# Performance work log

Hardware: AMD Instinct MI355X
Metric: run time of the kernel (lower is better)

Reference implementation:

```python
import jax, jax.numpy as jnp
import numpy as np

N = 50000      # nodes
E = 500000     # edges
MUL = 32       # multiplicity of 0e and 1o in node irreps
NUM_NEIGHBORS = 10.0
MIX = 0.15
INV3 = 1.0 / np.sqrt(3.0)  # sqrt(2*l3+1)*wigner_3j(1,1,0) = delta_ij/sqrt(3)


def setup_inputs() -> dict:
    key = jax.random.key(0)
    ks = jax.random.split(key, 16)
    f32 = jnp.float32
    node_input = jax.random.normal(ks[0], (N, 128), dtype=f32)  # 32x0e (32) + 32x1o (96)
    # edge_attr = spherical harmonics lmax=1, component normalization: Y0=1, |Y1|=sqrt(3)
    y1 = jax.random.normal(ks[1], (E, 3), dtype=f32)
    y1 = jnp.sqrt(3.0) * y1 / jnp.linalg.norm(y1, axis=1, keepdims=True)
    edge_attr = jnp.concatenate([jnp.ones((E, 1), f32), y1], axis=1)  # [E,4]
    edge_scalars = jax.random.uniform(ks[2], (E, 8), dtype=f32)       # radial embedding
    edge_src = jax.random.randint(ks[3], (E,), 0, N)
    edge_dst = jax.random.randint(ks[4], (E,), 0, N)
    rn = lambda k, s: jax.random.normal(k, s, dtype=f32)
    return {
        "node_input": node_input, "edge_attr": edge_attr, "edge_scalars": edge_scalars,
        "W1_s": rn(ks[5], (MUL, 2 * MUL)),  # first Linear, 0e block: 32 -> 64 (=feat 32 + self 32)
        "W1_v": rn(ks[6], (MUL, 2 * MUL)),  # first Linear, 1o block
        "M0": rn(ks[7], (8, 32)), "M1": rn(ks[8], (32, 32)),  # weight MLP (fc_neurons=[32,32])
        "Wtp0": rn(ks[9], (32, MUL)),   # path 0e x 0e -> 0e
        "Wtp1": rn(ks[10], (32, MUL)),  # path 0e x 1o -> 1o
        "Wtp2": rn(ks[11], (32, MUL)),  # path 1o x 0e -> 1o
        "Wtp3": rn(ks[12], (32, MUL)),  # path 1o x 1o -> 0e
        "W2_s": rn(ks[13], (2 * MUL, MUL)),  # final Linear, 0e: 64 -> 32
        "W2_v": rn(ks[14], (2 * MUL, MUL)),  # final Linear, 1o: 64 -> 32
        "edge_src": edge_src, "edge_dst": edge_dst,
    }


def _forward(node_input, edge_attr, edge_scalars, W1_s, W1_v, M0, M1,
             Wtp0, Wtp1, Wtp2, Wtp3, W2_s, W2_v, edge_src, edge_dst):
    n = node_input.shape[0]
    s = node_input[:, :MUL]                       # [N,32]  0e
    v = node_input[:, MUL:].reshape(n, MUL, 3)    # [N,32,3] 1o
    # Linear(node_input.irreps + irreps_out): per-irrep mixing, fan-in normalized
    s_all = (s @ W1_s) / jnp.sqrt(jnp.float32(MUL))                    # [N,64]
    v_all = jnp.einsum('nuk,uw->nwk', v, W1_v) / jnp.sqrt(jnp.float32(MUL))  # [N,64,3]
    feat_s, self_s = s_all[:, :MUL], s_all[:, MUL:]
    feat_v, self_v = v_all[:, :MUL], v_all[:, MUL:]

    # gather by edge source
    es = feat_s[edge_src]   # [E,32]
    ev = feat_v[edge_src]   # [E,32,3]
    y0 = edge_attr[:, 0]    # [E]
    y1 = edge_attr[:, 1:4]  # [E,3]

    # MLP on edge scalars -> per-edge, per-path 'uvu' weights (fan-in normalized)
    h = jax.nn.gelu(edge_scalars @ M0 / jnp.sqrt(jnp.float32(8)))
    h = jax.nn.gelu(h @ M1 / jnp.sqrt(jnp.float32(32)))                # [E,32]
    inv_sqrt_h = 1.0 / jnp.sqrt(jnp.float32(32))
    w0 = (h @ Wtp0) * inv_sqrt_h  # [E,32]
    w1 = (h @ Wtp1) * inv_sqrt_h
    w2 = (h @ Wtp2) * inv_sqrt_h
    w3 = (h @ Wtp3) * inv_sqrt_h

    # per-edge CG tensor product (4 'uvu' instructions)
    out0a = w0 * es * y0[:, None]                                    # 0e x 0e -> 0e
    out0b = w3 * jnp.einsum('euk,ek->eu', ev, y1) * INV3             # 1o x 1o -> 0e
    out1a = w1[:, :, None] * es[:, :, None] * y1[:, None, :]        # 0e x 1o -> 1o
    out1b = w2[:, :, None] * ev * y0[:, None, None]                 # 1o x 0e -> 1o
    out0 = jnp.concatenate([out0a, out0b], axis=1)                  # [E,64]  64x0e
    out1 = jnp.concatenate([out1a, out1b], axis=1)                  # [E,64,3] 64x1o

    # scatter-add to destination nodes, normalize by sqrt(num_neighbors)
    inv_deg = 1.0 / jnp.sqrt(jnp.float32(NUM_NEIGHBORS))
    ns = jax.ops.segment_sum(out0, edge_dst, num_segments=n) * inv_deg              # [N,64]
    nv = jax.ops.segment_sum(out1.reshape(-1, 2 * MUL * 3), edge_dst,
                             num_segments=n).reshape(n, 2 * MUL, 3) * inv_deg       # [N,64,3]

    # final per-irrep Linear to output irreps 32x0e + 32x1o
    conv_s = (ns @ W2_s) / jnp.sqrt(jnp.float32(2 * MUL))
    conv_v = jnp.einsum('nuk,uw->nwk', nv, W2_v) / jnp.sqrt(jnp.float32(2 * MUL))

    a = jnp.sqrt(jnp.float32(1.0 - MIX))
    b = jnp.sqrt(jnp.float32(MIX))
    out_s = a * self_s + b * conv_s                                  # [N,32]
    out_v = (a * self_v + b * conv_v).reshape(n, MUL * 3)            # [N,96]
    return jnp.concatenate([out_s, out_v], axis=1)                   # [N,128]


def reference(node_input, edge_attr, edge_scalars, W1_s, W1_v, M0, M1,
              Wtp0, Wtp1, Wtp2, Wtp3, W2_s, W2_v, edge_src, edge_dst):
    return _forward(node_input, edge_attr, edge_scalars, W1_s, W1_v, M0, M1,
                    Wtp0, Wtp1, Wtp2, Wtp3, W2_s, W2_v, edge_src, edge_dst)
```

## Files before the change

### kernel.cpp

```cpp
#include <hip/hip_runtime.h>
#include <math.h>

#define N_NODES 50000
#define N_EDGES 500000
#define NPB 16
#define GROUPS 8

__device__ __forceinline__ float gelu_fast(float x) {
    const float k0 = 0.7978845608028654f;
    const float k1 = 0.044715f;
    float z2 = 2.f * k0 * (x + k1 * x * x * x);
    float ez = __expf(z2);
    float th = 1.f - 2.f * __builtin_amdgcn_rcpf(ez + 1.f);
    return 0.5f * x * (1.f + th);
}

__device__ __forceinline__ unsigned short f2bf(float x) {
    unsigned int u = __float_as_uint(x);
    unsigned int r = (u + 0x7FFFu + ((u >> 16) & 1u)) >> 16;
    return (unsigned short)r;
}
__device__ __forceinline__ unsigned int pack2bf(float a, float b) {
    return (unsigned int)f2bf(a) | ((unsigned int)f2bf(b) << 16);
}
__device__ __forceinline__ float bf_lo(unsigned int w) {
    return __uint_as_float(w << 16);
}
__device__ __forceinline__ float bf_hi(unsigned int w) {
    return __uint_as_float(w & 0xffff0000u);
}

__device__ __forceinline__ void lds_add(float* p, float v) {
    unsigned int off = (unsigned int)(size_t)p;
    asm volatile("ds_add_f32 %0, %1" :: "v"(off), "v"(v) : "memory");
}

__global__ void node_pre(const float* __restrict__ node_input,
                         const float* __restrict__ W1_s,
                         const float* __restrict__ W1_v,
                         float* __restrict__ feat,
                         float* __restrict__ out) {
    __shared__ float lWs[32 * 64];
    __shared__ float lWv[32 * 64];
    for (int i = threadIdx.x; i < 2048; i += blockDim.x) {
        lWs[i] = W1_s[i];
        lWv[i] = W1_v[i];
    }
    __syncthreads();
    int n = blockIdx.x * blockDim.x + threadIdx.x;
    if (n >= N_NODES) return;
    const float inv_sqrt_mul = 0.17677669529663687f;
    const float a_mix = 0.9219544457292887f;

    float s[32];
#pragma unroll
    for (int u = 0; u < 32; ++u) s[u] = node_input[n * 128 + u];
#pragma unroll 4
    for (int w = 0; w < 64; ++w) {
        float acc = 0.f;
#pragma unroll
        for (int u = 0; u < 32; ++u) acc += s[u] * lWs[u * 64 + w];
        acc *= inv_sqrt_mul;
        if (w < 32) feat[(size_t)n * 128 + w * 4 + 0] = acc;
        else        out[n * 128 + (w - 32)] = a_mix * acc;
    }
#pragma unroll
    for (int k = 0; k < 3; ++k) {
        float vk[32];
#pragma unroll
        for (int u = 0; u < 32; ++u) vk[u] = node_input[n * 128 + 32 + u * 3 + k];
#pragma unroll 4
        for (int w = 0; w < 64; ++w) {
            float acc = 0.f;
#pragma unroll
            for (int u = 0; u < 32; ++u) acc += vk[u] * lWv[u * 64 + w];
            acc *= inv_sqrt_mul;
            if (w < 32) feat[(size_t)n * 128 + w * 4 + 1 + k] = acc;
            else        out[n * 128 + 32 + (w - 32) * 3 + k] = a_mix * acc;
        }
    }
}

__global__ void hist_kernel(const int* __restrict__ edge_dst, int* __restrict__ counts) {
    int e = blockIdx.x * blockDim.x + threadIdx.x;
    if (e < N_EDGES) atomicAdd(&counts[edge_dst[e]], 1);
}

__global__ void scan_kernel(const int* __restrict__ counts,
                            int* __restrict__ offsets,
                            int* __restrict__ cursor) {
    const int T = 1024;
    __shared__ int partial[T];
    int t = threadIdx.x;
    const int chunk = (N_NODES + T - 1) / T;
    int start = t * chunk;
    int end = start + chunk; if (end > N_NODES) end = N_NODES;
    if (start > N_NODES) start = N_NODES;
    int sum = 0;
    for (int i = start; i < end; ++i) sum += counts[i];
    partial[t] = sum;
    __syncthreads();
    for (int off = 1; off < T; off <<= 1) {
        int other = (t >= off) ? partial[t - off] : 0;
        __syncthreads();
        partial[t] += other;
        __syncthreads();
    }
    int run = (t == 0) ? 0 : partial[t - 1];
    for (int i = start; i < end; ++i) {
        offsets[i] = run;
        cursor[i] = run;
        run += counts[i];
    }
    if (t == T - 1) offsets[N_NODES] = run;
}

__global__ void scatter_kernel(const int* __restrict__ edge_src,
                               const int* __restrict__ edge_dst,
                               const float* __restrict__ edge_attr,
                               int* __restrict__ cursor,
                               float4* __restrict__ ySorted,
                               int4* __restrict__ sde) {
    int e = blockIdx.x * blockDim.x + threadIdx.x;
    if (e >= N_EDGES) return;
    int d = edge_dst[e];
    int pos = atomicAdd(&cursor[d], 1);
    ySorted[pos] = *(const float4*)(edge_attr + (size_t)e * 4);
    sde[pos] = make_int4(edge_src[e], d, e, 0);
}

__global__ void __launch_bounds__(256)
h_kernel(const float* __restrict__ edge_scalars,
         const float* __restrict__ M0,
         const float* __restrict__ M1,
         uint4* __restrict__ hOut) {
    __shared__ unsigned int stage[256 * 20];

    const int wv   = threadIdx.x >> 6;
    const int lane = threadIdx.x & 63;
    const int e0w  = blockIdx.x * 256 + wv * 64;
    int e = e0w + lane;
    int ec = e < N_EDGES ? e : N_EDGES - 1;

    const float inv_sqrt8  = 0.35355339059327373f;
    const float inv_sqrt32 = 0.17677669529663687f;

    const float4 s0 = *(const float4*)(edge_scalars + (size_t)ec * 8);
    const float4 s1 = *(const float4*)(edge_scalars + (size_t)ec * 8 + 4);

    float t[32];
#pragma unroll
    for (int u = 0; u < 32; ++u) {
        float acc = s0.x * M0[0 * 32 + u] + s0.y * M0[1 * 32 + u]
                  + s0.z * M0[2 * 32 + u] + s0.w * M0[3 * 32 + u]
                  + s1.x * M0[4 * 32 + u] + s1.y * M0[5 * 32 + u]
                  + s1.z * M0[6 * 32 + u] + s1.w * M0[7 * 32 + u];
        t[u] = gelu_fast(acc * inv_sqrt8);
    }
    float h[32];
#pragma unroll
    for (int u = 0; u < 32; ++u) {
        float acc = 0.f;
#pragma unroll
        for (int m = 0; m < 32; ++m) acc += t[m] * M1[m * 32 + u];
        h[u] = gelu_fast(acc * inv_sqrt32);
    }

    unsigned int* myrow = stage + threadIdx.x * 20;
#pragma unroll
    for (int c = 0; c < 4; ++c) {
        uint4 pk;
        pk.x = pack2bf(h[c * 8 + 0], h[c * 8 + 1]);
        pk.y = pack2bf(h[c * 8 + 2], h[c * 8 + 3]);
        pk.z = pack2bf(h[c * 8 + 4], h[c * 8 + 5]);
        pk.w = pack2bf(h[c * 8 + 6], h[c * 8 + 7]);
        *(uint4*)&myrow[c * 4] = pk;
    }
    asm volatile("s_waitcnt lgkmcnt(0)" ::: "memory");
#pragma unroll
    for (int p = 0; p < 4; ++p) {
        const int el = p * 16 + (lane >> 2);
        const int c  = lane & 3;
        const uint4 v = *(const uint4*)&stage[(wv * 64 + el) * 20 + c * 4];
        const int ge = e0w + el;
        if (ge < N_EDGES)
            hOut[(size_t)ge * 4 + c] = v;
    }
}

__global__ void __launch_bounds__(256)
conv_kernel(const uint4* __restrict__ hBuf,
            const float4* __restrict__ ySorted,
            const int4* __restrict__ sde,
            const int* __restrict__ offsets,
            const float* __restrict__ Wtp0,
            const float* __restrict__ Wtp1,
            const float* __restrict__ Wtp2,
            const float* __restrict__ Wtp3,
            const float* __restrict__ W2_s,
            const float* __restrict__ W2_v,
            const float* __restrict__ feat,
            float* __restrict__ out) {
    __shared__ float sacc[NPB * 256];
    for (int i = threadIdx.x; i < NPB * 256; i += blockDim.x) sacc[i] = 0.f;

    const int lane = threadIdx.x & 31;
    const int g = threadIdx.x >> 5;

    const float inv_sqrt32 = 0.17677669529663687f;
    unsigned int wA[32], wB[32];
#pragma unroll
    for (int j = 0; j < 32; ++j) {
        wA[j] = pack2bf(Wtp0[j * 32 + lane] * inv_sqrt32,
                        Wtp1[j * 32 + lane] * inv_sqrt32);
        wB[j] = pack2bf(Wtp2[j * 32 + lane] * inv_sqrt32,
                        Wtp3[j * 32 + lane] * inv_sqrt32);
    }
    __syncthreads();

    const int n0 = blockIdx.x * NPB;
    const int eb = offsets[n0];
    const int ee = offsets[n0 + NPB];
    const float INV3 = 0.5773502691896258f;
    const float4* feat4 = (const float4*)feat;

    const int total = ee - eb;
    const int per = (total + GROUPS - 1) / GROUPS;
    const int es = eb + g * per;
    int et = es + per; if (et > ee) et = ee;

    float r0 = 0.f, r1 = 0.f, r2 = 0.f, r3 = 0.f;
    float r4 = 0.f, r5 = 0.f, r6 = 0.f, r7 = 0.f;
    int cur = -1;

    for (int e = es; e < et; ++e) {
        const int4 sd = sde[e];
        const float4 yq = ySorted[e];
        const float4 f = feat4[(size_t)sd.x * 32 + lane];
        const uint4 hq0 = hBuf[(size_t)sd.z * 4 + 0];
        const uint4 hq1 = hBuf[(size_t)sd.z * 4 + 1];
        const uint4 hq2 = hBuf[(size_t)sd.z * 4 + 2];
        const uint4 hq3 = hBuf[(size_t)sd.z * 4 + 3];

        if (sd.y != cur) {
            if (cur >= 0) {
                float* ap = sacc + (cur - n0) * 256;
                lds_add(ap + lane, r0);
                lds_add(ap + 32 + lane, r1);
                lds_add(ap + 64 + lane * 3 + 0, r2);
                lds_add(ap + 64 + lane * 3 + 1, r3);
                lds_add(ap + 64 + lane * 3 + 2, r4);
                lds_add(ap + 160 + lane * 3 + 0, r5);
                lds_add(ap + 160 + lane * 3 + 1, r6);
                lds_add(ap + 160 + lane * 3 + 2, r7);
            }
            cur = sd.y;
            r0 = r1 = r2 = r3 = r4 = r5 = r6 = r7 = 0.f;
        }

        float w0 = 0.f, w1 = 0.f, w2 = 0.f, w3 = 0.f;
        unsigned int hw[16] = {hq0.x, hq0.y, hq0.z, hq0.w,
                               hq1.x, hq1.y, hq1.z, hq1.w,
                               hq2.x, hq2.y, hq2.z, hq2.w,
                               hq3.x, hq3.y, hq3.z, hq3.w};
#pragma unroll
        for (int k = 0; k < 16; ++k) {
            const float hlo = bf_lo(hw[k]);
            const float hhi = bf_hi(hw[k]);
            const unsigned int a0 = wA[2 * k],     b0 = wB[2 * k];
            const unsigned int a1 = wA[2 * k + 1], b1 = wB[2 * k + 1];
            w0 += hlo * bf_lo(a0); w1 += hlo * bf_hi(a0);
            w2 += hlo * bf_lo(b0); w3 += hlo * bf_hi(b0);
            w0 += hhi * bf_lo(a1); w1 += hhi * bf_hi(a1);
            w2 += hhi * bf_lo(b1); w3 += hhi * bf_hi(b1);
        }

        const float dvy = f.y * yq.y + f.z * yq.z + f.w * yq.w;
        const float w1es = w1 * f.x;
        const float w2y0 = w2 * yq.x;

        r0 += w0 * f.x * yq.x;
        r1 += w3 * dvy * INV3;
        r2 += w1es * yq.y;
        r3 += w1es * yq.z;
        r4 += w1es * yq.w;
        r5 += w2y0 * f.y;
        r6 += w2y0 * f.z;
        r7 += w2y0 * f.w;
    }
    if (cur >= 0) {
        float* ap = sacc + (cur - n0) * 256;
        lds_add(ap + lane, r0);
        lds_add(ap + 32 + lane, r1);
        lds_add(ap + 64 + lane * 3 + 0, r2);
        lds_add(ap + 64 + lane * 3 + 1, r3);
        lds_add(ap + 64 + lane * 3 + 2, r4);
        lds_add(ap + 160 + lane * 3 + 0, r5);
        lds_add(ap + 160 + lane * 3 + 1, r6);
        lds_add(ap + 160 + lane * 3 + 2, r7);
    }
    asm volatile("s_waitcnt lgkmcnt(0)" ::: "memory");
    __syncthreads();

    const float scale = 0.31622776601683794f * 0.125f * 0.3872983346207417f;
    for (int li = g; li < NPB; li += GROUPS) {
        const float* ap = sacc + li * 256;
        float cs = 0.f, cv0 = 0.f, cv1 = 0.f, cv2 = 0.f;
#pragma unroll 8
        for (int j = 0; j < 64; ++j) {
            const float as = ap[j];
            cs += as * __ldg(&W2_s[j * 32 + lane]);
            const float wv = __ldg(&W2_v[j * 32 + lane]);
            cv0 += ap[64 + 3 * j + 0] * wv;
            cv1 += ap[64 + 3 * j + 1] * wv;
            cv2 += ap[64 + 3 * j + 2] * wv;
        }
        float* o = out + (size_t)(n0 + li) * 128;
        o[lane]              += scale * cs;
        o[32 + lane * 3 + 0] += scale * cv0;
        o[32 + lane * 3 + 1] += scale * cv1;
        o[32 + lane * 3 + 2] += scale * cv2;
    }
}

extern "C" void kernel_launch(void* const* d_in, const int* in_sizes, int n_in,
                              void* d_out, int out_size, void* d_ws, size_t ws_size,
                              hipStream_t stream) {
    const float* node_input   = (const float*)d_in[0];
    const float* edge_attr    = (const float*)d_in[1];
    const float* edge_scalars = (const float*)d_in[2];
    const float* W1_s = (const float*)d_in[3];
    const float* W1_v = (const float*)d_in[4];
    const float* M0   = (const float*)d_in[5];
    const float* M1   = (const float*)d_in[6];
    const float* Wtp0 = (const float*)d_in[7];
    const float* Wtp1 = (const float*)d_in[8];
    const float* Wtp2 = (const float*)d_in[9];
    const float* Wtp3 = (const float*)d_in[10];
    const float* W2_s = (const float*)d_in[11];
    const float* W2_v = (const float*)d_in[12];
    const int* edge_src = (const int*)d_in[13];
    const int* edge_dst = (const int*)d_in[14];
    float* out = (float*)d_out;
    float* ws  = (float*)d_ws;

    float*  feat    = ws;
    float4* ySorted = (float4*)(feat + (size_t)N_NODES * 128);
    uint4*  hBuf    = (uint4*)(ySorted + N_EDGES);
    int4*   sde     = (int4*)(hBuf + (size_t)N_EDGES * 4);
    int*    counts  = (int*)(sde + N_EDGES);
    int*    offsets = counts + N_NODES;
    int*    cursor  = offsets + N_NODES + 1;

    hipMemsetAsync(counts, 0, N_NODES * sizeof(int), stream);

    node_pre<<<(N_NODES + 255) / 256, 256, 0, stream>>>(node_input, W1_s, W1_v,
                                                        feat, out);

    hist_kernel<<<(N_EDGES + 255) / 256, 256, 0, stream>>>(edge_dst, counts);
    scan_kernel<<<1, 1024, 0, stream>>>(counts, offsets, cursor);
    scatter_kernel<<<(N_EDGES + 255) / 256, 256, 0, stream>>>(edge_src, edge_dst,
                                                              edge_attr,
                                                              cursor, ySorted, sde);

    h_kernel<<<(N_EDGES + 255) / 256, 256, 0, stream>>>(edge_scalars, M0, M1, hBuf);

    conv_kernel<<<N_NODES / NPB, 256, 0, stream>>>(hBuf, ySorted, sde, offsets,
                                                   Wtp0, Wtp1, Wtp2, Wtp3,
                                                   W2_s, W2_v, feat, out);
}
```

Baseline: 561.9 us.

## Write edge MLP output in dst-sorted order and prefetch next edge in conv loop

The scatter kernel now records each edge's sorted position, and the h kernel writes its bf16 weights straight into dst-sorted slots. The conv kernel then reads h contiguously instead of gathering by original edge id, and the index record shrinks from int4 to int2. The conv loop also software-pipelines the loads of the next edge's data, and nodes per block drop from 16 to 8 for more blocks. The cost is scattered, uncoalesced 64-byte writes in the h kernel, plus extra registers from the prefetch.

```diff
diff --git a/kernel.cpp b/kernel.cpp
--- a/kernel.cpp
+++ b/kernel.cpp
@@ -3,7 +3,7 @@
 
 #define N_NODES 50000
 #define N_EDGES 500000
-#define NPB 16
+#define NPB 8
 #define GROUPS 8
 
 __device__ __forceinline__ float gelu_fast(float x) {
@@ -120,33 +120,32 @@
                                const float* __restrict__ edge_attr,
                                int* __restrict__ cursor,
                                float4* __restrict__ ySorted,
-                               int4* __restrict__ sde) {
+                               int2* __restrict__ srcdst,
+                               int* __restrict__ epos) {
     int e = blockIdx.x * blockDim.x + threadIdx.x;
     if (e >= N_EDGES) return;
     int d = edge_dst[e];
     int pos = atomicAdd(&cursor[d], 1);
     ySorted[pos] = *(const float4*)(edge_attr + (size_t)e * 4);
-    sde[pos] = make_int4(edge_src[e], d, e, 0);
+    srcdst[pos] = make_int2(edge_src[e], d);
+    epos[e] = pos;
 }
 
 __global__ void __launch_bounds__(256)
 h_kernel(const float* __restrict__ edge_scalars,
+         const int* __restrict__ epos,
          const float* __restrict__ M0,
          const float* __restrict__ M1,
-         uint4* __restrict__ hOut) {
-    __shared__ unsigned int stage[256 * 20];
-
-    const int wv   = threadIdx.x >> 6;
-    const int lane = threadIdx.x & 63;
-    const int e0w  = blockIdx.x * 256 + wv * 64;
-    int e = e0w + lane;
-    int ec = e < N_EDGES ? e : N_EDGES - 1;
+         uint4* __restrict__ hSorted) {
+    const int e = blockIdx.x * blockDim.x + threadIdx.x;
+    if (e >= N_EDGES) return;
 
     const float inv_sqrt8  = 0.35355339059327373f;
     const float inv_sqrt32 = 0.17677669529663687f;
 
-    const float4 s0 = *(const float4*)(edge_scalars + (size_t)ec * 8);
-    const float4 s1 = *(const float4*)(edge_scalars + (size_t)ec * 8 + 4);
+    const float4 s0 = *(const float4*)(edge_scalars + (size_t)e * 8);
+    const float4 s1 = *(const float4*)(edge_scalars + (size_t)e * 8 + 4);
+    const int pos = epos[e];
 
     float t[32];
 #pragma unroll
@@ -166,7 +165,7 @@
         h[u] = gelu_fast(acc * inv_sqrt32);
     }
 
-    unsigned int* myrow = stage + threadIdx.x * 20;
+    uint4* dst = hSorted + (size_t)pos * 4;
 #pragma unroll
     for (int c = 0; c < 4; ++c) {
         uint4 pk;
@@ -174,24 +173,14 @@
         pk.y = pack2bf(h[c * 8 + 2], h[c * 8 + 3]);
         pk.z = pack2bf(h[c * 8 + 4], h[c * 8 + 5]);
         pk.w = pack2bf(h[c * 8 + 6], h[c * 8 + 7]);
-        *(uint4*)&myrow[c * 4] = pk;
-    }
-    asm volatile("s_waitcnt lgkmcnt(0)" ::: "memory");
-#pragma unroll
-    for (int p = 0; p < 4; ++p) {
-        const int el = p * 16 + (lane >> 2);
-        const int c  = lane & 3;
-        const uint4 v = *(const uint4*)&stage[(wv * 64 + el) * 20 + c * 4];
-        const int ge = e0w + el;
-        if (ge < N_EDGES)
-            hOut[(size_t)ge * 4 + c] = v;
+        dst[c] = pk;
     }
 }
 
 __global__ void __launch_bounds__(256)
-conv_kernel(const uint4* __restrict__ hBuf,
+conv_kernel(const uint4* __restrict__ hSorted,
             const float4* __restrict__ ySorted,
-            const int4* __restrict__ sde,
+            const int2* __restrict__ srcdst,
             const int* __restrict__ offsets,
             const float* __restrict__ Wtp0,
             const float* __restrict__ Wtp1,
@@ -233,77 +222,96 @@
     float r4 = 0.f, r5 = 0.f, r6 = 0.f, r7 = 0.f;
     int cur = -1;
 
-    for (int e = es; e < et; ++e) {
-        const int4 sd = sde[e];
-        const float4 yq = ySorted[e];
-        const float4 f = feat4[(size_t)sd.x * 32 + lane];
-        const uint4 hq0 = hBuf[(size_t)sd.z * 4 + 0];
-        const uint4 hq1 = hBuf[(size_t)sd.z * 4 + 1];
-        const uint4 hq2 = hBuf[(size_t)sd.z * 4 + 2];
-        const uint4 hq3 = hBuf[(size_t)sd.z * 4 + 3];
-
-        if (sd.y != cur) {
-            if (cur >= 0) {
-                float* ap = sacc + (cur - n0) * 256;
-                lds_add(ap + lane, r0);
-                lds_add(ap + 32 + lane, r1);
-                lds_add(ap + 64 + lane * 3 + 0, r2);
-                lds_add(ap + 64 + lane * 3 + 1, r3);
-                lds_add(ap + 64 + lane * 3 + 2, r4);
-                lds_add(ap + 160 + lane * 3 + 0, r5);
-                lds_add(ap + 160 + lane * 3 + 1, r6);
-                lds_add(ap + 160 + lane * 3 + 2, r7);
+    if (es < et) {
+        const int last = et - 1;
+        int2 sd = srcdst[es];
+        float4 yq = ySorted[es];
+        uint4 h0 = hSorted[(size_t)es * 4 + 0];
+        uint4 h1 = hSorted[(size_t)es * 4 + 1];
+        uint4 h2 = hSorted[(size_t)es * 4 + 2];
+        uint4 h3 = hSorted[(size_t)es * 4 + 3];
+        float4 f = feat4[(size_t)sd.x * 32 + lane];
+        int e1 = es + 1 <= last ? es + 1 : last;
+        int2 sdN = srcdst[e1];
+
+        for (int e = es; e < et; ++e) {
+            const int ep1 = e + 1 <= last ? e + 1 : last;
+            const int ep2 = e + 2 <= last ? e + 2 : last;
+            float4 yqN = ySorted[ep1];
+            uint4 h0N = hSorted[(size_t)ep1 * 4 + 0];
+            uint4 h1N = hSorted[(size_t)ep1 * 4 + 1];
+            uint4 h2N = hSorted[(size_t)ep1 * 4 + 2];
+            uint4 h3N = hSorted[(size_t)ep1 * 4 + 3];
+            float4 fN = feat4[(size_t)sdN.x * 32 + lane];
+            int2 sdNN = srcdst[ep2];
+
+            if (sd.y != cur) {
+                if (cur >= 0) {
+                    float* ap = sacc + (cur - n0) * 256;
+                    lds_add(ap + lane, r0);
+                    lds_add(ap + 32 + lane, r1);
+                    lds_add(ap + 64 + lane * 3 + 0, r2);
+                    lds_add(ap + 64 + lane * 3 + 1, r3);
+                    lds_add(ap + 64 + lane * 3 + 2, r4);
+                    lds_add(ap + 160 + lane * 3 + 0, r5);
+                    lds_add(ap + 160 + lane * 3 + 1, r6);
+                    lds_add(ap + 160 + lane * 3 + 2, r7);
+                }
+                cur = sd.y;
+                r0 = r1 = r2 = r3 = r4 = r5 = r6 = r7 = 0.f;
             }
-            cur = sd.y;
-            r0 = r1 = r2 = r3 = r4 = r5 = r6 = r7 = 0.f;
+
+            float w0 = 0.f, w1 = 0.f, w2 = 0.f, w3 = 0.f;
+            const unsigned int hw[16] = {h0.x, h0.y, h0.z, h0.w,
+                                         h1.x, h1.y, h1.z, h1.w,
+                                         h2.x, h2.y, h2.z, h2.w,
+                                         h3.x, h3.y, h3.z, h3.w};
+#pragma unroll
+            for (int k = 0; k < 16; ++k) {
+                const float hlo = bf_lo(hw[k]);
+                const float hhi = bf_hi(hw[k]);
+                const unsigned int a0 = wA[2 * k],     b0 = wB[2 * k];
+                const unsigned int a1 = wA[2 * k + 1], b1 = wB[2 * k + 1];
+                w0 += hlo * bf_lo(a0); w1 += hlo * bf_hi(a0);
+                w2 += hlo * bf_lo(b0); w3 += hlo * bf_hi(b0);
+                w0 += hhi * bf_lo(a1); w1 += hhi * bf_hi(a1);
+                w2 += hhi * bf_lo(b1); w3 += hhi * bf_hi(b1);
+            }
+
+            const float dvy = f.y * yq.y + f.z * yq.z + f.w * yq.w;
+            const float w1es = w1 * f.x;
+            const float w2y0 = w2 * yq.x;
+
+            r0 += w0 * f.x * yq.x;
+            r1 += w3 * dvy * INV3;
+            r2 += w1es * yq.y;
+            r3 += w1es * yq.z;
+            r4 += w1es * yq.w;
+            r5 += w2y0 * f.y;
+            r6 += w2y0 * f.z;
+            r7 += w2y0 * f.w;
+
+            sd = sdN; sdN = sdNN;
+            yq = yqN; h0 = h0N; h1 = h1N; h2 = h2N; h3 = h3N; f = fN;
         }
-
-        float w0 = 0.f, w1 = 0.f, w2 = 0.f, w3 = 0.f;
-        unsigned int hw[16] = {hq0.x, hq0.y, hq0.z, hq0.w,
-                               hq1.x, hq1.y, hq1.z, hq1.w,
-                               hq2.x, hq2.y, hq2.z, hq2.w,
-                               hq3.x, hq3.y, hq3.z, hq3.w};
-#pragma unroll
-        for (int k = 0; k < 16; ++k) {
-            const float hlo = bf_lo(hw[k]);
-            const float hhi = bf_hi(hw[k]);
-            const unsigned int a0 = wA[2 * k],     b0 = wB[2 * k];
-            const unsigned int a1 = wA[2 * k + 1], b1 = wB[2 * k + 1];
-            w0 += hlo * bf_lo(a0); w1 += hlo * bf_hi(a0);
-            w2 += hlo * bf_lo(b0); w3 += hlo * bf_hi(b0);
-            w0 += hhi * bf_lo(a1); w1 += hhi * bf_hi(a1);
-            w2 += hhi * bf_lo(b1); w3 += hhi * bf_hi(b1);
+        if (cur >= 0) {
+            float* ap = sacc + (cur - n0) * 256;
+            lds_add(ap + lane, r0);
+            lds_add(ap + 32 + lane, r1);
+            lds_add(ap + 64 + lane * 3 + 0, r2);
+            lds_add(ap + 64 + lane * 3 + 1, r3);
+            lds_add(ap + 64 + lane * 3 + 2, r4);
+            lds_add(ap + 160 + lane * 3 + 0, r5);
+            lds_add(ap + 160 + lane * 3 + 1, r6);
+            lds_add(ap + 160 + lane * 3 + 2, r7);
         }
-
-        const float dvy = f.y * yq.y + f.z * yq.z + f.w * yq.w;
-        const float w1es = w1 * f.x;
-        const float w2y0 = w2 * yq.x;
-
-        r0 += w0 * f.x * yq.x;
-        r1 += w3 * dvy * INV3;
-        r2 += w1es * yq.y;
-        r3 += w1es * yq.z;
-        r4 += w1es * yq.w;
-        r5 += w2y0 * f.y;
-        r6 += w2y0 * f.z;
-        r7 += w2y0 * f.w;
-    }
-    if (cur >= 0) {
-        float* ap = sacc + (cur - n0) * 256;
-        lds_add(ap + lane, r0);
-        lds_add(ap + 32 + lane, r1);
-        lds_add(ap + 64 + lane * 3 + 0, r2);
-        lds_add(ap + 64 + lane * 3 + 1, r3);
-        lds_add(ap + 64 + lane * 3 + 2, r4);
-        lds_add(ap + 160 + lane * 3 + 0, r5);
-        lds_add(ap + 160 + lane * 3 + 1, r6);
-        lds_add(ap + 160 + lane * 3 + 2, r7);
     }
     asm volatile("s_waitcnt lgkmcnt(0)" ::: "memory");
     __syncthreads();
 
     const float scale = 0.31622776601683794f * 0.125f * 0.3872983346207417f;
-    for (int li = g; li < NPB; li += GROUPS) {
+    {
+        const int li = g;
         const float* ap = sacc + li * 256;
         float cs = 0.f, cv0 = 0.f, cv1 = 0.f, cv2 = 0.f;
 #pragma unroll 8
@@ -346,9 +354,10 @@
 
     float*  feat    = ws;
     float4* ySorted = (float4*)(feat + (size_t)N_NODES * 128);
-    uint4*  hBuf    = (uint4*)(ySorted + N_EDGES);
-    int4*   sde     = (int4*)(hBuf + (size_t)N_EDGES * 4);
-    int*    counts  = (int*)(sde + N_EDGES);
+    uint4*  hSorted = (uint4*)(ySorted + N_EDGES);
+    int2*   srcdst  = (int2*)(hSorted + (size_t)N_EDGES * 4);
+    int*    epos    = (int*)(srcdst + N_EDGES);
+    int*    counts  = epos + N_EDGES;
     int*    offsets = counts + N_NODES;
     int*    cursor  = offsets + N_NODES + 1;
 
@@ -360,12 +369,13 @@
     hist_kernel<<<(N_EDGES + 255) / 256, 256, 0, stream>>>(edge_dst, counts);
     scan_kernel<<<1, 1024, 0, stream>>>(counts, offsets, cursor);
     scatter_kernel<<<(N_EDGES + 255) / 256, 256, 0, stream>>>(edge_src, edge_dst,
-                                                              edge_attr,
-                                                              cursor, ySorted, sde);
-
-    h_kernel<<<(N_EDGES + 255) / 256, 256, 0, stream>>>(edge_scalars, M0, M1, hBuf);
-
-    conv_kernel<<<N_NODES / NPB, 256, 0, stream>>>(hBuf, ySorted, sde, offsets,
+                                                              edge_attr, cursor,
+                                                              ySorted, srcdst, epos);
+
+    h_kernel<<<(N_EDGES + 255) / 256, 256, 0, stream>>>(edge_scalars, epos,
+                                                        M0, M1, hSorted);
+
+    conv_kernel<<<N_NODES / NPB, 256, 0, stream>>>(hSorted, ySorted, srcdst, offsets,
                                                    Wtp0, Wtp1, Wtp2, Wtp3,
                                                    W2_s, W2_v, feat, out);
 }
```

After: 572.3 us. Within noise of the previous version (+1.8%).
